# Performance work log

Hardware: AMD Instinct MI355X
Metric: run time of the kernel (lower is better)

Reference implementation:

```python
import jax, jax.numpy as jnp
import numpy as np

N_NODES = 100000
N_EDGES = 1600000
F_IN, HIDDEN, N_CLASS = 256, 64, 2


def _gcn_conv(x, W, b, src, dst, norm, n):
    # PyG GCNConv: linear (no bias) -> normalized scatter-add -> bias
    h = x @ W                                  # [N, out]
    msg = h[src] * norm[:, None]               # gather + scale, [E+N, out]
    agg = jax.ops.segment_sum(msg, dst, num_segments=n)
    return agg + b


def setup_inputs() -> dict:
    key = jax.random.key(0)
    ks = jax.random.split(key, 8)
    x = jax.random.normal(ks[0], (N_NODES, F_IN), dtype=jnp.float32)
    edge_index = jax.random.randint(ks[1], (2, N_EDGES), 0, N_NODES, dtype=jnp.int32)
    W1 = jax.random.normal(ks[2], (F_IN, HIDDEN), dtype=jnp.float32) / np.sqrt(F_IN).astype(np.float32)
    b1 = jnp.zeros((HIDDEN,), dtype=jnp.float32)
    W2 = jax.random.normal(ks[3], (HIDDEN, HIDDEN), dtype=jnp.float32) / np.sqrt(HIDDEN).astype(np.float32)
    b2 = jnp.zeros((HIDDEN,), dtype=jnp.float32)
    W3 = jax.random.normal(ks[4], (HIDDEN, N_CLASS), dtype=jnp.float32) / np.sqrt(HIDDEN).astype(np.float32)
    b3 = jnp.zeros((N_CLASS,), dtype=jnp.float32)
    return {"x": x, "edge_index": edge_index, "W1": W1, "b1": b1, "W2": W2, "b2": b2, "W3": W3, "b3": b3}


def reference(x, edge_index, W1, b1, W2, b2, W3, b3):
    n = x.shape[0]
    # add self-loops (GCNConv default)
    loops = jnp.arange(n, dtype=edge_index.dtype)
    src = jnp.concatenate([edge_index[0], loops])
    dst = jnp.concatenate([edge_index[1], loops])
    # symmetric normalization D^-1/2 A_hat D^-1/2
    deg = jax.ops.segment_sum(jnp.ones_like(src, dtype=x.dtype), dst, num_segments=n)
    deg_inv_sqrt = jnp.where(deg > 0, jax.lax.rsqrt(jnp.maximum(deg, 1.0)), 0.0)
    norm = deg_inv_sqrt[src] * deg_inv_sqrt[dst]
    # layer 1 + relu (dropout is identity in eval mode)
    h = jax.nn.relu(_gcn_conv(x, W1, b1, src, dst, norm, n))
    # layer 2 + relu
    h = jax.nn.relu(_gcn_conv(h, W2, b2, src, dst, norm, n))
    # output layer + log_softmax
    h = _gcn_conv(h, W3, b3, src, dst, norm, n)
    return jax.nn.log_softmax(h, axis=1)
```

## Files before the change

kernel.cpp:

```cpp
#include <hip/hip_runtime.h>
#include <math.h>

#define F_IN 256
#define HID  64
#define BSH  8
#define BSPAN 256
#define CHUNK 16384
#define NBK_MAX 512

__global__ __launch_bounds__(256) void k_hist(const int* __restrict__ dst,
                                              int* __restrict__ cntT,
                                              int E, int NCH, int NBK) {
    __shared__ int hist[NBK_MAX];
    int t = threadIdx.x, c = blockIdx.x;
    hist[t] = 0; hist[t + 256] = 0;
    __syncthreads();
    int base = c * CHUNK;
#pragma unroll 4
    for (int j = 0; j < CHUNK / 256; j++) {
        int e = base + j * 256 + t;
        if (e < E) atomicAdd(&hist[dst[e] >> BSH], 1);
    }
    __syncthreads();
    for (int b = t; b < NBK; b += 256) cntT[b * NCH + c] = hist[b];
}

__global__ __launch_bounds__(256) void k_scanA(const int* __restrict__ cntT,
                                               int* __restrict__ off,
                                               int* __restrict__ partials, int S) {
    __shared__ int sh[256];
    int tid = threadIdx.x;
    int base = blockIdx.x * 1024 + tid * 4;
    int v[4];
    int s = 0;
#pragma unroll
    for (int j = 0; j < 4; j++) {
        int idx = base + j;
        v[j] = (idx < S) ? cntT[idx] : 0;
        s += v[j];
    }
    sh[tid] = s;
    __syncthreads();
    int mysum = s;
    for (int o = 1; o < 256; o <<= 1) {
        int tv = (tid >= o) ? sh[tid - o] : 0;
        __syncthreads();
        sh[tid] += tv;
        __syncthreads();
    }
    int pref = sh[tid] - mysum;
#pragma unroll
    for (int j = 0; j < 4; j++) {
        int idx = base + j;
        if (idx < S) off[idx] = pref;
        pref += v[j];
    }
    if (tid == 255) partials[blockIdx.x] = sh[255];
}

__global__ void k_scanB(int* __restrict__ partials, int* __restrict__ off,
                        int nblk, int S) {
    if (blockIdx.x == 0 && threadIdx.x == 0) {
        int run = 0;
        for (int b = 0; b < nblk; b++) { int t = partials[b]; partials[b] = run; run += t; }
        off[S] = run;
    }
}

__global__ void k_scanC(int* __restrict__ off, const int* __restrict__ partials, int S) {
    int i = blockIdx.x * blockDim.x + threadIdx.x;
    if (i < S) off[i] += partials[i >> 10];
}

__global__ __launch_bounds__(256) void k_sortwrite(const int* __restrict__ src,
                                                   const int* __restrict__ dst,
                                                   const int* __restrict__ off,
                                                   int* __restrict__ ebuf,
                                                   int E, int NCH, int NBK) {
    __shared__ int cur[NBK_MAX];
    int t = threadIdx.x, c = blockIdx.x;
    for (int b = t; b < NBK; b += 256) cur[b] = off[b * NCH + c];
    __syncthreads();
    int base = c * CHUNK;
#pragma unroll 4
    for (int j = 0; j < CHUNK / 256; j++) {
        int e = base + j * 256 + t;
        if (e < E) {
            int s = src[e];
            int d = dst[e];
            int pos = atomicAdd(&cur[d >> BSH], 1);
            ebuf[pos] = (s << BSH) | (d & (BSPAN - 1));
        }
    }
}

__global__ __launch_bounds__(256) void k_bucket_csr(const int* __restrict__ off,
                                                    const int* __restrict__ ebuf,
                                                    int* __restrict__ rp,
                                                    float* __restrict__ dinv,
                                                    int* __restrict__ esrc,
                                                    int N, int NCH, int NBK) {
    __shared__ int cnt[BSPAN];
    __shared__ int sh[BSPAN];
    int b = blockIdx.x, t = threadIdx.x;
    int base = off[b * NCH];
    int end  = off[(b + 1) * NCH];

    cnt[t] = 0;
    __syncthreads();
    for (int i = base + t; i < end; i += 256) atomicAdd(&cnt[ebuf[i] & (BSPAN - 1)], 1);
    __syncthreads();

    int c = cnt[t];
    sh[t] = c;
    __syncthreads();
    for (int o = 1; o < 256; o <<= 1) {
        int tv = (t >= o) ? sh[t - o] : 0;
        __syncthreads();
        sh[t] += tv;
        __syncthreads();
    }
    int excl = sh[t] - c;

    int node = (b << BSH) + t;
    if (node < N) {
        rp[node] = base + excl;
        dinv[node] = rsqrtf((float)(1 + c));
    }
    if (b == NBK - 1 && t == 0) rp[N] = end;
    __syncthreads();

    cnt[t] = base + excl;
    __syncthreads();
    for (int i = base + t; i < end; i += 256) {
        int v = ebuf[i];
        int p = atomicAdd(&cnt[v & (BSPAN - 1)], 1);
        esrc[p] = v >> BSH;
    }
}

template <int K>
__global__ __launch_bounds__(256) void k_gemm64(const float* __restrict__ A,
                                                const float* __restrict__ B,
                                                const float* __restrict__ dinv,
                                                float* __restrict__ C, int nrows) {
    __shared__ float As[16][68];
    __shared__ float Bs[16][64];

    int tid = threadIdx.x;
    int tx = tid & 15;
    int ty = tid >> 4;
    int row0 = blockIdx.x * 64;

    int arow = tid >> 2;
    int ak   = (tid & 3) * 4;
    int brow = tid >> 4;
    int bcol = (tid & 15) * 4;

    float acc[4][4] = {};

    for (int k0 = 0; k0 < K; k0 += 16) {
        int gr = row0 + arow;
        float4 av = make_float4(0.f, 0.f, 0.f, 0.f);
        if (gr < nrows) av = *(const float4*)(A + (size_t)gr * K + k0 + ak);
        float4 bv = *(const float4*)(B + (size_t)(k0 + brow) * 64 + bcol);
        __syncthreads();
        As[ak + 0][arow] = av.x;
        As[ak + 1][arow] = av.y;
        As[ak + 2][arow] = av.z;
        As[ak + 3][arow] = av.w;
        *(float4*)&Bs[brow][bcol] = bv;
        __syncthreads();
#pragma unroll
        for (int kk = 0; kk < 16; kk++) {
            float4 a = *(const float4*)&As[kk][4 * ty];
            float4 bq = *(const float4*)&Bs[kk][4 * tx];
            acc[0][0] += a.x * bq.x; acc[0][1] += a.x * bq.y; acc[0][2] += a.x * bq.z; acc[0][3] += a.x * bq.w;
            acc[1][0] += a.y * bq.x; acc[1][1] += a.y * bq.y; acc[1][2] += a.y * bq.z; acc[1][3] += a.y * bq.w;
            acc[2][0] += a.z * bq.x; acc[2][1] += a.z * bq.y; acc[2][2] += a.z * bq.z; acc[2][3] += a.z * bq.w;
            acc[3][0] += a.w * bq.x; acc[3][1] += a.w * bq.y; acc[3][2] += a.w * bq.z; acc[3][3] += a.w * bq.w;
        }
    }
#pragma unroll
    for (int i = 0; i < 4; i++) {
        int row = row0 + 4 * ty + i;
        if (row < nrows) {
            float di = dinv[row];
            float4 o = make_float4(acc[i][0] * di, acc[i][1] * di, acc[i][2] * di, acc[i][3] * di);
            *(float4*)(C + (size_t)row * 64 + 4 * tx) = o;
        }
    }
}

template <int MODE>
__global__ __launch_bounds__(256) void k_agg64(const float* __restrict__ hs,
                                               const float* __restrict__ dinv,
                                               const int* __restrict__ rp,
                                               const int* __restrict__ esrc,
                                               const float* __restrict__ bias,
                                               const float* __restrict__ W3,
                                               float* __restrict__ out, int n) {
    int lane = threadIdx.x & 63;
    int nid = blockIdx.x * 4 + (threadIdx.x >> 6);
    if (nid >= n) return;
    nid = __builtin_amdgcn_readfirstlane(nid);

    float dii = dinv[nid];
    int e0 = rp[nid];
    int e1 = rp[nid + 1];

    float a0 = hs[(size_t)nid * 64 + lane];
    float a1 = 0.f, a2 = 0.f, a3 = 0.f, a4 = 0.f, a5 = 0.f, a6 = 0.f, a7 = 0.f;

    for (int e = e0; e < e1; e += 8) {
        int last = e1 - 1;
        int i0 = esrc[e];
        int i1 = esrc[min(e + 1, last)];
        int i2 = esrc[min(e + 2, last)];
        int i3 = esrc[min(e + 3, last)];
        int i4 = esrc[min(e + 4, last)];
        int i5 = esrc[min(e + 5, last)];
        int i6 = esrc[min(e + 6, last)];
        int i7 = esrc[min(e + 7, last)];
        float v0 = hs[(size_t)i0 * 64 + lane];
        float v1 = hs[(size_t)i1 * 64 + lane];
        float v2 = hs[(size_t)i2 * 64 + lane];
        float v3 = hs[(size_t)i3 * 64 + lane];
        float v4 = hs[(size_t)i4 * 64 + lane];
        float v5 = hs[(size_t)i5 * 64 + lane];
        float v6 = hs[(size_t)i6 * 64 + lane];
        float v7 = hs[(size_t)i7 * 64 + lane];
        a0 += v0;
        a1 += (e + 1 <= last) ? v1 : 0.f;
        a2 += (e + 2 <= last) ? v2 : 0.f;
        a3 += (e + 3 <= last) ? v3 : 0.f;
        a4 += (e + 4 <= last) ? v4 : 0.f;
        a5 += (e + 5 <= last) ? v5 : 0.f;
        a6 += (e + 6 <= last) ? v6 : 0.f;
        a7 += (e + 7 <= last) ? v7 : 0.f;
    }

    float acc = ((a0 + a1) + (a2 + a3)) + ((a4 + a5) + (a6 + a7));
    acc = acc * dii + bias[lane];
    acc = fmaxf(acc, 0.f);

    if (MODE == 0) {
        out[(size_t)nid * 64 + lane] = acc;
    } else {
        float2 w3 = ((const float2*)W3)[lane];
        float p0 = acc * w3.x;
        float p1 = acc * w3.y;
#pragma unroll
        for (int o = 32; o > 0; o >>= 1) {
            p0 += __shfl_xor(p0, o, 64);
            p1 += __shfl_xor(p1, o, 64);
        }
        if (lane == 0) ((float2*)out)[nid] = make_float2(p0 * dii, p1 * dii);
    }
}

__global__ __launch_bounds__(256) void k_final(const float2* __restrict__ h3s,
                                               const float* __restrict__ dinv,
                                               const int* __restrict__ rp,
                                               const int* __restrict__ esrc,
                                               const float* __restrict__ b3,
                                               float* __restrict__ out, int n) {
    int i = blockIdx.x * blockDim.x + threadIdx.x;
    if (i >= n) return;
    float dii = dinv[i];
    float2 h = h3s[i];
    float ax = h.x, ay = h.y;
    float bx = 0.f, by = 0.f, cx = 0.f, cy = 0.f, dx = 0.f, dy = 0.f;
    int e0 = rp[i], e1 = rp[i + 1];
    for (int e = e0; e < e1; e += 4) {
        int last = e1 - 1;
        int s0 = esrc[e];
        int s1 = esrc[min(e + 1, last)];
        int s2 = esrc[min(e + 2, last)];
        int s3 = esrc[min(e + 3, last)];
        float2 v0 = h3s[s0];
        float2 v1 = h3s[s1];
        float2 v2 = h3s[s2];
        float2 v3 = h3s[s3];
        ax += v0.x; ay += v0.y;
        bx += (e + 1 <= last) ? v1.x : 0.f; by += (e + 1 <= last) ? v1.y : 0.f;
        cx += (e + 2 <= last) ? v2.x : 0.f; cy += (e + 2 <= last) ? v2.y : 0.f;
        dx += (e + 3 <= last) ? v3.x : 0.f; dy += (e + 3 <= last) ? v3.y : 0.f;
    }
    float l0 = ((ax + bx) + (cx + dx)) * dii + b3[0];
    float l1 = ((ay + by) + (cy + dy)) * dii + b3[1];
    float m = fmaxf(l0, l1);
    float lse = m + logf(expf(l0 - m) + expf(l1 - m));
    ((float2*)out)[i] = make_float2(l0 - lse, l1 - lse);
}

extern "C" void kernel_launch(void* const* d_in, const int* in_sizes, int n_in,
                              void* d_out, int out_size, void* d_ws, size_t ws_size,
                              hipStream_t stream) {
    const float* x   = (const float*)d_in[0];
    const int*   ei  = (const int*)d_in[1];
    const float* W1  = (const float*)d_in[2];
    const float* b1  = (const float*)d_in[3];
    const float* W2  = (const float*)d_in[4];
    const float* b2  = (const float*)d_in[5];
    const float* W3  = (const float*)d_in[6];
    const float* b3  = (const float*)d_in[7];
    float* out = (float*)d_out;

    const int N = in_sizes[0] / F_IN;
    const int E = in_sizes[1] / 2;
    const int* src = ei;
    const int* dst = ei + E;

    const int NBK = (N + BSPAN - 1) / BSPAN;
    const int NCH = (E + CHUNK - 1) / CHUNK;
    const int S   = NBK * NCH;

    char* p = (char*)d_ws;
    auto alloc = [&](size_t bytes) -> void* {
        void* r = (void*)p;
        p += (bytes + 255) & ~(size_t)255;
        return r;
    };
    int*   cntT     = (int*)alloc((size_t)S * 4);
    int*   off      = (int*)alloc((size_t)(S + 1) * 4);
    int*   partials = (int*)alloc(4096);
    int*   ebuf     = (int*)alloc((size_t)E * 4);
    int*   esrc     = (int*)alloc((size_t)E * 4);
    int*   rp       = (int*)alloc((size_t)(N + 1) * 4);
    float* dinv     = (float*)alloc((size_t)N * 4);
    float* bufA     = (float*)alloc((size_t)N * HID * 4);
    float* bufB     = (float*)alloc((size_t)N * HID * 4);
    float* h3       = (float*)alloc((size_t)N * 2 * 4);

    const int T = 256;
    int scanBlocks = (S + 1023) / 1024;

    k_hist<<<NCH, T, 0, stream>>>(dst, cntT, E, NCH, NBK);
    k_scanA<<<scanBlocks, T, 0, stream>>>(cntT, off, partials, S);
    k_scanB<<<1, 64, 0, stream>>>(partials, off, scanBlocks, S);
    k_scanC<<<(S + T - 1) / T, T, 0, stream>>>(off, partials, S);
    k_sortwrite<<<NCH, T, 0, stream>>>(src, dst, off, ebuf, E, NCH, NBK);
    k_bucket_csr<<<NBK, T, 0, stream>>>(off, ebuf, rp, dinv, esrc, N, NCH, NBK);

    int gemmBlocks = (N + 63) / 64;
    k_gemm64<F_IN><<<gemmBlocks, T, 0, stream>>>(x, W1, dinv, bufA, N);
    k_agg64<0><<<(N + 3) / 4, T, 0, stream>>>(bufA, dinv, rp, esrc, b1, nullptr, bufB, N);

    k_gemm64<HID><<<gemmBlocks, T, 0, stream>>>(bufB, W2, dinv, bufA, N);
    k_agg64<1><<<(N + 3) / 4, T, 0, stream>>>(bufA, dinv, rp, esrc, b2, W3, h3, N);

    k_final<<<(N + T - 1) / T, T, 0, stream>>>((const float2*)h3, dinv, rp, esrc, b3, out, N);
}
```

Measured before the change: 419.3 us.

## Replace FP32 SIMT GEMMs with split-bf16 MFMA GEMMs using pre-transposed weights

Swaps the shared-memory FP32 tiled GEMM for a matrix-core kernel using mfma_f32_16x16x32_bf16. Each wave computes a 16x64 tile, and precision is kept near FP32 by splitting both operands into high and low bf16 parts and summing three products. A new small kernel transposes and splits W1 and W2 into bf16 hi/lo buffers. The cost is extra conversion work on the A operand per k-step, plus uncoalesced scalar stores of C and direct global loads of B without LDS reuse.

```diff
diff --git a/kernel.cpp b/kernel.cpp
--- a/kernel.cpp
+++ b/kernel.cpp
@@ -7,6 +7,9 @@
 #define BSPAN 256
 #define CHUNK 16384
 #define NBK_MAX 512
+
+typedef __bf16 bf16x8 __attribute__((ext_vector_type(8)));
+typedef float  floatx4 __attribute__((ext_vector_type(4)));
 
 __global__ __launch_bounds__(256) void k_hist(const int* __restrict__ dst,
                                               int* __restrict__ cntT,
@@ -139,55 +142,80 @@
     }
 }
 
+__global__ __launch_bounds__(256) void k_prepw(const float* __restrict__ W1,
+                                               __bf16* __restrict__ w1h, __bf16* __restrict__ w1l,
+                                               const float* __restrict__ W2,
+                                               __bf16* __restrict__ w2h, __bf16* __restrict__ w2l) {
+    int t = threadIdx.x + blockIdx.x * blockDim.x;
+    for (int idx = t; idx < 64 * 256; idx += 256 * 8) {
+        int c = idx >> 8, k = idx & 255;
+        float w = W1[k * 64 + c];
+        __bf16 h = (__bf16)w;
+        w1h[idx] = h;
+        w1l[idx] = (__bf16)(w - (float)h);
+    }
+    for (int idx = t; idx < 64 * 64; idx += 256 * 8) {
+        int c = idx >> 6, k = idx & 63;
+        float w = W2[k * 64 + c];
+        __bf16 h = (__bf16)w;
+        w2h[idx] = h;
+        w2l[idx] = (__bf16)(w - (float)h);
+    }
+}
+
 template <int K>
-__global__ __launch_bounds__(256) void k_gemm64(const float* __restrict__ A,
-                                                const float* __restrict__ B,
-                                                const float* __restrict__ dinv,
-                                                float* __restrict__ C, int nrows) {
-    __shared__ float As[16][68];
-    __shared__ float Bs[16][64];
-
-    int tid = threadIdx.x;
-    int tx = tid & 15;
-    int ty = tid >> 4;
-    int row0 = blockIdx.x * 64;
-
-    int arow = tid >> 2;
-    int ak   = (tid & 3) * 4;
-    int brow = tid >> 4;
-    int bcol = (tid & 15) * 4;
-
-    float acc[4][4] = {};
-
-    for (int k0 = 0; k0 < K; k0 += 16) {
-        int gr = row0 + arow;
-        float4 av = make_float4(0.f, 0.f, 0.f, 0.f);
-        if (gr < nrows) av = *(const float4*)(A + (size_t)gr * K + k0 + ak);
-        float4 bv = *(const float4*)(B + (size_t)(k0 + brow) * 64 + bcol);
-        __syncthreads();
-        As[ak + 0][arow] = av.x;
-        As[ak + 1][arow] = av.y;
-        As[ak + 2][arow] = av.z;
-        As[ak + 3][arow] = av.w;
-        *(float4*)&Bs[brow][bcol] = bv;
-        __syncthreads();
-#pragma unroll
-        for (int kk = 0; kk < 16; kk++) {
-            float4 a = *(const float4*)&As[kk][4 * ty];
-            float4 bq = *(const float4*)&Bs[kk][4 * tx];
-            acc[0][0] += a.x * bq.x; acc[0][1] += a.x * bq.y; acc[0][2] += a.x * bq.z; acc[0][3] += a.x * bq.w;
-            acc[1][0] += a.y * bq.x; acc[1][1] += a.y * bq.y; acc[1][2] += a.y * bq.z; acc[1][3] += a.y * bq.w;
-            acc[2][0] += a.z * bq.x; acc[2][1] += a.z * bq.y; acc[2][2] += a.z * bq.z; acc[2][3] += a.z * bq.w;
-            acc[3][0] += a.w * bq.x; acc[3][1] += a.w * bq.y; acc[3][2] += a.w * bq.z; acc[3][3] += a.w * bq.w;
-        }
-    }
+__global__ __launch_bounds__(256) void k_gemm_mfma(const float* __restrict__ A,
+                                                   const __bf16* __restrict__ BtH,
+                                                   const __bf16* __restrict__ BtL,
+                                                   const float* __restrict__ dinv,
+                                                   float* __restrict__ C, int nrows) {
+    int wave = threadIdx.x >> 6;
+    int lane = threadIdx.x & 63;
+    int m = lane & 15;
+    int q = lane >> 4;
+    int row0 = blockIdx.x * 64 + wave * 16;
+    int arow = row0 + m;
+    bool rvalid = arow < nrows;
+    const float* ap = A + (size_t)arow * K + q * 8;
+
+    floatx4 acc[4] = {{0.f, 0.f, 0.f, 0.f}, {0.f, 0.f, 0.f, 0.f},
+                      {0.f, 0.f, 0.f, 0.f}, {0.f, 0.f, 0.f, 0.f}};
+
+    for (int k0 = 0; k0 < K; k0 += 32) {
+        float4 f0 = make_float4(0.f, 0.f, 0.f, 0.f);
+        float4 f1 = make_float4(0.f, 0.f, 0.f, 0.f);
+        if (rvalid) {
+            f0 = *(const float4*)(ap + k0);
+            f1 = *(const float4*)(ap + k0 + 4);
+        }
+        float af[8] = {f0.x, f0.y, f0.z, f0.w, f1.x, f1.y, f1.z, f1.w};
+        bf16x8 ah, al;
+#pragma unroll
+        for (int j = 0; j < 8; j++) {
+            __bf16 h = (__bf16)af[j];
+            ah[j] = h;
+            al[j] = (__bf16)(af[j] - (float)h);
+        }
+#pragma unroll
+        for (int c = 0; c < 4; c++) {
+            const __bf16* bp = BtH + (size_t)(c * 16 + m) * K + k0 + q * 8;
+            const __bf16* bq = BtL + (size_t)(c * 16 + m) * K + k0 + q * 8;
+            bf16x8 bh = *(const bf16x8*)bp;
+            bf16x8 bl = *(const bf16x8*)bq;
+            acc[c] = __builtin_amdgcn_mfma_f32_16x16x32_bf16(ah, bh, acc[c], 0, 0, 0);
+            acc[c] = __builtin_amdgcn_mfma_f32_16x16x32_bf16(al, bh, acc[c], 0, 0, 0);
+            acc[c] = __builtin_amdgcn_mfma_f32_16x16x32_bf16(ah, bl, acc[c], 0, 0, 0);
+        }
+    }
+
 #pragma unroll
     for (int i = 0; i < 4; i++) {
-        int row = row0 + 4 * ty + i;
-        if (row < nrows) {
-            float di = dinv[row];
-            float4 o = make_float4(acc[i][0] * di, acc[i][1] * di, acc[i][2] * di, acc[i][3] * di);
-            *(float4*)(C + (size_t)row * 64 + 4 * tx) = o;
+        int r = row0 + q * 4 + i;
+        if (r < nrows) {
+            float di = dinv[r];
+#pragma unroll
+            for (int c = 0; c < 4; c++)
+                C[(size_t)r * 64 + c * 16 + m] = acc[c][i] * di;
         }
     }
 }
@@ -322,19 +350,25 @@
         p += (bytes + 255) & ~(size_t)255;
         return r;
     };
-    int*   cntT     = (int*)alloc((size_t)S * 4);
-    int*   off      = (int*)alloc((size_t)(S + 1) * 4);
-    int*   partials = (int*)alloc(4096);
-    int*   ebuf     = (int*)alloc((size_t)E * 4);
-    int*   esrc     = (int*)alloc((size_t)E * 4);
-    int*   rp       = (int*)alloc((size_t)(N + 1) * 4);
-    float* dinv     = (float*)alloc((size_t)N * 4);
-    float* bufA     = (float*)alloc((size_t)N * HID * 4);
-    float* bufB     = (float*)alloc((size_t)N * HID * 4);
-    float* h3       = (float*)alloc((size_t)N * 2 * 4);
+    int*    cntT     = (int*)alloc((size_t)S * 4);
+    int*    off      = (int*)alloc((size_t)(S + 1) * 4);
+    int*    partials = (int*)alloc(4096);
+    int*    ebuf     = (int*)alloc((size_t)E * 4);
+    int*    esrc     = (int*)alloc((size_t)E * 4);
+    int*    rp       = (int*)alloc((size_t)(N + 1) * 4);
+    float*  dinv     = (float*)alloc((size_t)N * 4);
+    float*  bufA     = (float*)alloc((size_t)N * HID * 4);
+    float*  bufB     = (float*)alloc((size_t)N * HID * 4);
+    float*  h3       = (float*)alloc((size_t)N * 2 * 4);
+    __bf16* w1h      = (__bf16*)alloc(64 * 256 * 2);
+    __bf16* w1l      = (__bf16*)alloc(64 * 256 * 2);
+    __bf16* w2h      = (__bf16*)alloc(64 * 64 * 2);
+    __bf16* w2l      = (__bf16*)alloc(64 * 64 * 2);
 
     const int T = 256;
     int scanBlocks = (S + 1023) / 1024;
+
+    k_prepw<<<8, T, 0, stream>>>(W1, w1h, w1l, W2, w2h, w2l);
 
     k_hist<<<NCH, T, 0, stream>>>(dst, cntT, E, NCH, NBK);
     k_scanA<<<scanBlocks, T, 0, stream>>>(cntT, off, partials, S);
@@ -344,10 +378,10 @@
     k_bucket_csr<<<NBK, T, 0, stream>>>(off, ebuf, rp, dinv, esrc, N, NCH, NBK);
 
     int gemmBlocks = (N + 63) / 64;
-    k_gemm64<F_IN><<<gemmBlocks, T, 0, stream>>>(x, W1, dinv, bufA, N);
+    k_gemm_mfma<F_IN><<<gemmBlocks, T, 0, stream>>>(x, w1h, w1l, dinv, bufA, N);
     k_agg64<0><<<(N + 3) / 4, T, 0, stream>>>(bufA, dinv, rp, esrc, b1, nullptr, bufB, N);
 
-    k_gemm64<HID><<<gemmBlocks, T, 0, stream>>>(bufB, W2, dinv, bufA, N);
+    k_gemm_mfma<HID><<<gemmBlocks, T, 0, stream>>>(bufB, w2h, w2l, dinv, bufA, N);
     k_agg64<1><<<(N + 3) / 4, T, 0, stream>>>(bufA, dinv, rp, esrc, b2, W3, h3, N);
 
     k_final<<<(N + T - 1) / T, T, 0, stream>>>((const float2*)h3, dinv, rp, esrc, b3, out, N);
```

Result: slower. 449.7 us (+7.3%).
